# Optimization experiments

Hardware: AMD Instinct MI355X
Metric: run time of the kernel (lower is better)

The kernel has to match this reference:

```python
import jax, jax.numpy as jnp
import numpy as np

B, N, M = 64, 1025, 1024          # N = M + 1 (node 0 is the zero-padding node)
TREE_FEAT = 96
QVEC = 95                          # sum(range(10)) + 10*5
IN_CH = TREE_FEAT + 32             # tree features + q_conv output
EPS = 1e-5


def _tree_conv(x, idx, W, b):
    # x: (B, C, N); idx: (B, 3M) child-triple indices into node axis
    g = jnp.take_along_axis(x, idx[:, None, :], axis=2)        # (B, C, 3M)
    Bn, C, L = g.shape
    g = g.reshape(Bn, C, L // 3, 3)                            # (B, C, M, 3)
    out = jnp.einsum('bcmk,ock->bom', g, W) + b[None, :, None] # Conv1d k=3 s=3
    zero = jnp.zeros((Bn, W.shape[0], 1), out.dtype)           # re-prepend zero node
    return jnp.concatenate([zero, out], axis=2)                # (B, O, M+1)


def _tree_norm(x):
    # TreeLayerNorm: per-sample mean/std over (channels, nodes); torch.std is unbiased
    mean = jnp.mean(x, axis=(1, 2), keepdims=True)
    std = jnp.std(x, axis=(1, 2), keepdims=True, ddof=1)
    return (x - mean) / (std + EPS)


def setup_inputs() -> dict:
    key = jax.random.key(0)
    ks = jax.random.split(key, 17)
    p = lambda k, s: jax.random.normal(k, s, dtype=jnp.float32) * 0.05
    return {
        'q_vecs': jax.random.normal(ks[0], (B, QVEC), dtype=jnp.float32),
        'trees': jax.random.normal(ks[1], (B, N, TREE_FEAT), dtype=jnp.float32),
        'idxes': jax.random.randint(ks[2], (B, 3 * M), 0, N),
        # q_conv: Linear(95,64) -> Linear(64,128) -> Linear(128,64) -> Linear(64,32)
        'Wq1': p(ks[3], (QVEC, 64)),  'bq1': jnp.zeros((64,), jnp.float32),
        'Wq2': p(ks[4], (64, 128)),   'bq2': jnp.zeros((128,), jnp.float32),
        'Wq3': p(ks[5], (128, 64)),   'bq3': jnp.zeros((64,), jnp.float32),
        'Wq4': p(ks[6], (64, 32)),    'bq4': jnp.zeros((32,), jnp.float32),
        # tree_conv kernels: (out, in, 3)
        'Wc1': p(ks[7], (512, IN_CH, 3)), 'bc1': jnp.zeros((512,), jnp.float32),
        'Wc2': p(ks[8], (256, 512, 3)),   'bc2': jnp.zeros((256,), jnp.float32),
        'Wc3': p(ks[9], (128, 256, 3)),   'bc3': jnp.zeros((128,), jnp.float32),
    }


def reference(q_vecs, trees, idxes,
              Wq1, bq1, Wq2, bq2, Wq3, bq3, Wq4, bq4,
              Wc1, bc1, Wc2, bc2, Wc3, bc3):
    # q_conv: 4 stacked linears (no nonlinearity between them in the source)
    q = q_vecs @ Wq1 + bq1
    q = q @ Wq2 + bq2
    q = q @ Wq3 + bq3
    q = q @ Wq4 + bq4                                    # (B, 32)

    Bn, Nn = trees.shape[:2]
    q_rep = jnp.broadcast_to(q[:, None, :], (Bn, Nn, q.shape[-1]))
    aug = jnp.concatenate([trees, q_rep], axis=2)        # (B, N, IN_CH)
    x = jnp.transpose(aug, (0, 2, 1))                    # (B, IN_CH, N)

    x = _tree_conv(x, idxes, Wc1, bc1)
    x = jax.nn.leaky_relu(_tree_norm(x), negative_slope=0.01)
    x = _tree_conv(x, idxes, Wc2, bc2)
    x = jax.nn.leaky_relu(_tree_norm(x), negative_slope=0.01)
    x = _tree_conv(x, idxes, Wc3, bc3)
    x = _tree_norm(x)
    return jnp.max(x, axis=2)                            # DynamicPooling -> (B, 128)
```

## Files before the change

kernel.cpp:

```cpp
#include <hip/hip_runtime.h>
#include <hip/hip_bf16.h>

typedef __attribute__((ext_vector_type(8))) short short8;
typedef __attribute__((ext_vector_type(4))) float f32x4;

#define EPSV 1e-5f

__device__ __forceinline__ float bf2f(ushort u){
  union { uint i; float f; } x; x.i = ((uint)u) << 16; return x.f;
}
__device__ __forceinline__ ushort f2bf(float f){
  union { float f; uint i; } x; x.f = f;
  uint r = (x.i + 0x7FFFu + ((x.i >> 16) & 1u)) >> 16;
  return (ushort)r;
}

__global__ void init_kernel(ushort* x1, float* stats, int* maxbuf){
  int i = blockIdx.x * 256 + threadIdx.x;
  if (i < 384)  stats[i] = 0.f;
  if (i < 8192) maxbuf[i] = 0;
  if (i < 32768){ int b = i >> 9, c = i & 511; x1[(size_t)b*1025*512 + c] = 0; }
}

__global__ void zero2_kernel(ushort* x2){
  int i = blockIdx.x * 256 + threadIdx.x;
  int b = i >> 8, c = i & 255;
  x2[(size_t)b*1025*256 + c] = 0;
}

__global__ void qconv_kernel(const float* __restrict__ qv,
    const float* __restrict__ W1, const float* __restrict__ b1,
    const float* __restrict__ W2, const float* __restrict__ b2,
    const float* __restrict__ W3, const float* __restrict__ b3,
    const float* __restrict__ W4, const float* __restrict__ b4,
    float* __restrict__ qout){
  __shared__ float v0[96], h1[64], h2[128], h3[64];
  int b = blockIdx.x, t = threadIdx.x;
  if (t < 95) v0[t] = qv[b*95 + t];
  __syncthreads();
  if (t < 64){ float s = b1[t]; for (int i=0;i<95;i++)  s += v0[i]*W1[i*64 + t];  h1[t]=s; }
  __syncthreads();
  if (t < 128){ float s = b2[t]; for (int i=0;i<64;i++)  s += h1[i]*W2[i*128 + t]; h2[t]=s; }
  __syncthreads();
  if (t < 64){ float s = b3[t]; for (int i=0;i<128;i++) s += h2[i]*W3[i*64 + t];  h3[t]=s; }
  __syncthreads();
  if (t < 32){ float s = b4[t]; for (int i=0;i<64;i++)  s += h3[i]*W4[i*32 + t];  qout[b*32 + t]=s; }
}

__global__ void aug_kernel(const float* __restrict__ trees, const float* __restrict__ q,
                           ushort* __restrict__ aug){
  int n = blockIdx.x;
  int b = blockIdx.y;
  int c = threadIdx.x;
  float v = (c < 96) ? trees[((size_t)b*1025 + n)*96 + c] : q[b*32 + (c - 96)];
  aug[(((size_t)b*1025 + n) << 7) + c] = f2bf(v);
}

__global__ void prepw_kernel(const float* __restrict__ wc, ushort* __restrict__ wt,
                             int O, int C){
  int i = blockIdx.x * 256 + threadIdx.x;
  int total = O * 3 * C;
  if (i >= total) return;
  int o  = i / (3*C);
  int K  = i - o*3*C;
  int kp = K / C;
  int c  = K - kp*C;
  wt[i] = f2bf(wc[(o*C + c)*3 + kp]);
}

template<int CIN, int GY, bool DO_MAX>
__global__ __launch_bounds__(256) void conv_kernel(
    const ushort* __restrict__ xin, const ushort* __restrict__ wt,
    const float* __restrict__ bias, const int* __restrict__ idxes,
    ushort* __restrict__ xout, float* __restrict__ stats, int* __restrict__ maxbuf){
  constexpr int K3   = 3 * CIN;
  constexpr int NT   = K3 / 32;
  constexpr int COUT = GY * 128;
  constexpr int NWG  = 8 * GY * 64;

  const int bid  = blockIdx.x;
  const int wu   = (bid & 7) * (NWG >> 3) + (bid >> 3);
  const int m0   = (wu & 7) * 128;
  const int rest = wu >> 3;
  const int o0   = (rest % GY) * 128;
  const int b    = rest / GY;

  const int t = threadIdx.x;
  const int lane = t & 63, wid = t >> 6;
  const int WM = (wid & 1) * 64, WO = (wid >> 1) * 64;
  const int fr = lane & 15, fg = lane >> 4;
  const int fc = (fg ^ ((fr >> 1) & 3)) * 8;

  __shared__ __align__(16) union {
    struct { ushort A[2][128][32]; ushort B[2][128][32]; } s;
    ushort stage[128][132];
  } sh;
  __shared__ int idx_s[384];

  for (int i = t; i < 384; i += 256) idx_s[i] = idxes[b*3072 + m0*3 + i];
  __syncthreads();

  const int r = t >> 1, h = t & 1, sx = (r >> 1) & 3;
  const int p0 = ((2*h)     ^ sx) * 8;
  const int p1 = ((2*h + 1) ^ sx) * 8;
  const int n0 = idx_s[r*3 + 0], n1 = idx_s[r*3 + 1], n2 = idx_s[r*3 + 2];
  const ushort* xb   = xin + (size_t)b * 1025 * CIN;
  const ushort* wrow = wt + (size_t)(o0 + r) * K3 + h*16;

  uint4 ra0, ra1, rb0, rb1;
  auto GLOAD = [&](int ch){
    const int k0 = ch * 32;
    const int kp = k0 / CIN;
    const int c0 = k0 - kp * CIN;
    const int node = (kp == 0) ? n0 : (kp == 1) ? n1 : n2;
    const ushort* sa = xb + (size_t)node * CIN + c0 + h*16;
    ra0 = *reinterpret_cast<const uint4*>(sa);
    ra1 = *reinterpret_cast<const uint4*>(sa + 8);
    const ushort* sb = wrow + k0;
    rb0 = *reinterpret_cast<const uint4*>(sb);
    rb1 = *reinterpret_cast<const uint4*>(sb + 8);
  };
  auto DSW = [&](int bf){
    *reinterpret_cast<uint4*>(&sh.s.A[bf][r][p0]) = ra0;
    *reinterpret_cast<uint4*>(&sh.s.A[bf][r][p1]) = ra1;
    *reinterpret_cast<uint4*>(&sh.s.B[bf][r][p0]) = rb0;
    *reinterpret_cast<uint4*>(&sh.s.B[bf][r][p1]) = rb1;
  };

  f32x4 acc[4][4] = {};

  GLOAD(0);
  DSW(0);
  __syncthreads();

  for (int ch = 0; ch < NT; ++ch){
    if (ch + 1 < NT) GLOAD(ch + 1);
    const int cur = ch & 1;
    short8 af[4], bf4[4];
    #pragma unroll
    for (int i = 0; i < 4; ++i){
      af[i]  = *reinterpret_cast<const short8*>(&sh.s.A[cur][WM + i*16 + fr][fc]);
      bf4[i] = *reinterpret_cast<const short8*>(&sh.s.B[cur][WO + i*16 + fr][fc]);
    }
    __builtin_amdgcn_s_setprio(1);
    #pragma unroll
    for (int mf = 0; mf < 4; ++mf)
      #pragma unroll
      for (int nf = 0; nf < 4; ++nf)
        acc[mf][nf] = __builtin_amdgcn_mfma_f32_16x16x32_bf16(af[mf], bf4[nf], acc[mf][nf], 0, 0, 0);
    __builtin_amdgcn_s_setprio(0);
    if (ch + 1 < NT){
      DSW(cur ^ 1);
      __syncthreads();
    }
  }

  float bsv[4];
  #pragma unroll
  for (int nf = 0; nf < 4; ++nf) bsv[nf] = bias[o0 + WO + nf*16 + fr];
  float lsum = 0.f, lsq = 0.f;
  float cmax[4] = { -1e30f, -1e30f, -1e30f, -1e30f };
  #pragma unroll
  for (int mf = 0; mf < 4; ++mf)
    #pragma unroll
    for (int nf = 0; nf < 4; ++nf)
      #pragma unroll
      for (int i = 0; i < 4; ++i){
        float v = acc[mf][nf][i] + bsv[nf];
        lsum += v; lsq += v*v;
        if (DO_MAX) cmax[nf] = fmaxf(cmax[nf], v);
        else acc[mf][nf][i] = v;
      }
  #pragma unroll
  for (int off = 1; off < 64; off <<= 1){
    lsum += __shfl_xor(lsum, off);
    lsq  += __shfl_xor(lsq,  off);
  }
  if (lane == 0){
    atomicAdd(&stats[b],      lsum);
    atomicAdd(&stats[64 + b], lsq);
  }
  if (DO_MAX){
    #pragma unroll
    for (int nf = 0; nf < 4; ++nf){
      float v = cmax[nf];
      v = fmaxf(v, __shfl_xor(v, 16));
      v = fmaxf(v, __shfl_xor(v, 32));
      if (lane < 16)
        atomicMax(&maxbuf[b*COUT + o0 + WO + nf*16 + fr], __float_as_int(v));
    }
  } else {
    __syncthreads();
    #pragma unroll
    for (int mf = 0; mf < 4; ++mf)
      #pragma unroll
      for (int nf = 0; nf < 4; ++nf)
        #pragma unroll
        for (int i = 0; i < 4; ++i)
          sh.stage[WM + mf*16 + fg*4 + i][WO + nf*16 + fr] = f2bf(acc[mf][nf][i]);
    __syncthreads();
    #pragma unroll
    for (int it = 0; it < 16; ++it){
      int row = it*8 + (t >> 5);
      int col = (t & 31) * 4;
      uint2 v = *reinterpret_cast<const uint2*>(&sh.stage[row][col]);
      *reinterpret_cast<uint2*>(xout + ((size_t)(b*1025 + 1 + m0 + row))*COUT + o0 + col) = v;
    }
  }
}

__global__ void norm_kernel(ushort* __restrict__ x, const float* __restrict__ st,
                            float cnt, int nvec_per_b){
  int b = blockIdx.y;
  int j = blockIdx.x * 256 + threadIdx.x;
  if (j >= nvec_per_b) return;
  float sum = st[b], sq = st[64 + b];
  float mean = sum / cnt;
  float var  = fmaxf((sq - sum*sum/cnt) / (cnt - 1.f), 0.f);
  float rs   = 1.f / (sqrtf(var) + EPSV);
  ushort* p = x + ((size_t)b * nvec_per_b + j) * 8;
  union { uint4 v; ushort u[8]; } d;
  d.v = *reinterpret_cast<const uint4*>(p);
  #pragma unroll
  for (int k = 0; k < 8; ++k){
    float f = bf2f(d.u[k]);
    f = (f - mean) * rs;
    f = (f >= 0.f) ? f : 0.01f * f;
    d.u[k] = f2bf(f);
  }
  *reinterpret_cast<uint4*>(p) = d.v;
}

__global__ void final_kernel(const int* __restrict__ maxbuf, const float* __restrict__ st,
                             float* __restrict__ out){
  int i = blockIdx.x * 256 + threadIdx.x;
  int b = i >> 7;
  const float cnt = 131200.f;
  float sum = st[b], sq = st[64 + b];
  float mean = sum / cnt;
  float var  = fmaxf((sq - sum*sum/cnt) / (cnt - 1.f), 0.f);
  float rs   = 1.f / (sqrtf(var) + EPSV);
  out[i] = (__int_as_float(maxbuf[i]) - mean) * rs;
}

static constexpr size_t SZ_X1  = (size_t)64*1025*512*2;
static constexpr size_t SZ_X2  = (size_t)64*1025*256*2;
static constexpr size_t OFF_X1 = 0;
static constexpr size_t OFF_X2 = OFF_X1 + SZ_X1;
static constexpr size_t OFF_AUG = OFF_X2;
static constexpr size_t OFF_WT1 = OFF_X2 + SZ_X2;
static constexpr size_t OFF_WT2 = OFF_WT1 + (size_t)512*384*2;
static constexpr size_t OFF_WT3 = OFF_WT2 + (size_t)256*1536*2;
static constexpr size_t OFF_Q   = OFF_WT3 + (size_t)128*768*2;
static constexpr size_t OFF_ST  = OFF_Q + (size_t)64*32*4;
static constexpr size_t OFF_MAX = OFF_ST + (size_t)384*4;

extern "C" void kernel_launch(void* const* d_in, const int* in_sizes, int n_in,
                              void* d_out, int out_size, void* d_ws, size_t ws_size,
                              hipStream_t stream){
  const float* q_vecs = (const float*)d_in[0];
  const float* trees  = (const float*)d_in[1];
  const int*   idxes  = (const int*)  d_in[2];
  const float* Wq1 = (const float*)d_in[3];  const float* bq1 = (const float*)d_in[4];
  const float* Wq2 = (const float*)d_in[5];  const float* bq2 = (const float*)d_in[6];
  const float* Wq3 = (const float*)d_in[7];  const float* bq3 = (const float*)d_in[8];
  const float* Wq4 = (const float*)d_in[9];  const float* bq4 = (const float*)d_in[10];
  const float* Wc1 = (const float*)d_in[11]; const float* bc1 = (const float*)d_in[12];
  const float* Wc2 = (const float*)d_in[13]; const float* bc2 = (const float*)d_in[14];
  const float* Wc3 = (const float*)d_in[15]; const float* bc3 = (const float*)d_in[16];
  float* out = (float*)d_out;
  char* ws = (char*)d_ws;

  ushort* x1    = (ushort*)(ws + OFF_X1);
  ushort* x2    = (ushort*)(ws + OFF_X2);
  ushort* aug   = (ushort*)(ws + OFF_AUG);
  ushort* wt1   = (ushort*)(ws + OFF_WT1);
  ushort* wt2   = (ushort*)(ws + OFF_WT2);
  ushort* wt3   = (ushort*)(ws + OFF_WT3);
  float*  qbuf  = (float*) (ws + OFF_Q);
  float*  stats = (float*) (ws + OFF_ST);
  int*    maxb  = (int*)   (ws + OFF_MAX);

  init_kernel<<<128, 256, 0, stream>>>(x1, stats, maxb);
  qconv_kernel<<<64, 128, 0, stream>>>(q_vecs, Wq1,bq1, Wq2,bq2, Wq3,bq3, Wq4,bq4, qbuf);
  aug_kernel<<<dim3(1025, 64), 128, 0, stream>>>(trees, qbuf, aug);
  prepw_kernel<<<(512*384 + 255)/256, 256, 0, stream>>>(Wc1, wt1, 512, 128);
  prepw_kernel<<<(256*1536 + 255)/256, 256, 0, stream>>>(Wc2, wt2, 256, 512);
  prepw_kernel<<<(128*768 + 255)/256, 256, 0, stream>>>(Wc3, wt3, 128, 256);

  conv_kernel<128, 4, false><<<2048, 256, 0, stream>>>(aug, wt1, bc1, idxes, x1, stats +   0, nullptr);
  zero2_kernel<<<64, 256, 0, stream>>>(x2);
  norm_kernel<<<dim3((65600 + 255)/256, 64), 256, 0, stream>>>(x1, stats +   0, 524800.f, 65600);
  conv_kernel<512, 2, false><<<1024, 256, 0, stream>>>(x1,  wt2, bc2, idxes, x2, stats + 128, nullptr);
  norm_kernel<<<dim3((32800 + 255)/256, 64), 256, 0, stream>>>(x2, stats + 128, 262400.f, 32800);
  conv_kernel<256, 1, true ><<<512, 256, 0, stream>>>(x2,  wt3, bc3, idxes, nullptr, stats + 256, maxb);
  final_kernel<<<32, 256, 0, stream>>>(maxb, stats + 256, out);
}
```

Baseline: 276.4 us.

## Deepen conv GEMM prefetch to two chunks ahead with dual register buffers

```diff
diff --git a/kernel.cpp b/kernel.cpp
--- a/kernel.cpp
+++ b/kernel.cpp
@@ -75,6 +75,7 @@
     ushort* __restrict__ xout, float* __restrict__ stats, int* __restrict__ maxbuf){
   constexpr int K3   = 3 * CIN;
   constexpr int NT   = K3 / 32;
+  constexpr int LOG2 = (CIN == 128) ? 7 : (CIN == 256) ? 8 : 9;
   constexpr int COUT = GY * 128;
   constexpr int NWG  = 8 * GY * 64;
 
@@ -105,37 +106,51 @@
   const int p1 = ((2*h + 1) ^ sx) * 8;
   const int n0 = idx_s[r*3 + 0], n1 = idx_s[r*3 + 1], n2 = idx_s[r*3 + 2];
   const ushort* xb   = xin + (size_t)b * 1025 * CIN;
+  const ushort* pA0  = xb + (size_t)n0 * CIN + h*16;
+  const ushort* pA1  = xb + (size_t)n1 * CIN + h*16;
+  const ushort* pA2  = xb + (size_t)n2 * CIN + h*16;
   const ushort* wrow = wt + (size_t)(o0 + r) * K3 + h*16;
 
-  uint4 ra0, ra1, rb0, rb1;
-  auto GLOAD = [&](int ch){
+  uint4 a00, a01, b00, b01;
+  uint4 a10, a11, b10, b11;
+
+  auto GLOAD0 = [&](int ch){
     const int k0 = ch * 32;
-    const int kp = k0 / CIN;
-    const int c0 = k0 - kp * CIN;
-    const int node = (kp == 0) ? n0 : (kp == 1) ? n1 : n2;
-    const ushort* sa = xb + (size_t)node * CIN + c0 + h*16;
-    ra0 = *reinterpret_cast<const uint4*>(sa);
-    ra1 = *reinterpret_cast<const uint4*>(sa + 8);
+    const int kp = k0 >> LOG2;
+    const int c0 = k0 - (kp << LOG2);
+    const ushort* sa = ((kp == 0) ? pA0 : (kp == 1) ? pA1 : pA2) + c0;
+    a00 = *reinterpret_cast<const uint4*>(sa);
+    a01 = *reinterpret_cast<const uint4*>(sa + 8);
     const ushort* sb = wrow + k0;
-    rb0 = *reinterpret_cast<const uint4*>(sb);
-    rb1 = *reinterpret_cast<const uint4*>(sb + 8);
-  };
-  auto DSW = [&](int bf){
-    *reinterpret_cast<uint4*>(&sh.s.A[bf][r][p0]) = ra0;
-    *reinterpret_cast<uint4*>(&sh.s.A[bf][r][p1]) = ra1;
-    *reinterpret_cast<uint4*>(&sh.s.B[bf][r][p0]) = rb0;
-    *reinterpret_cast<uint4*>(&sh.s.B[bf][r][p1]) = rb1;
+    b00 = *reinterpret_cast<const uint4*>(sb);
+    b01 = *reinterpret_cast<const uint4*>(sb + 8);
+  };
+  auto GLOAD1 = [&](int ch){
+    const int k0 = ch * 32;
+    const int kp = k0 >> LOG2;
+    const int c0 = k0 - (kp << LOG2);
+    const ushort* sa = ((kp == 0) ? pA0 : (kp == 1) ? pA1 : pA2) + c0;
+    a10 = *reinterpret_cast<const uint4*>(sa);
+    a11 = *reinterpret_cast<const uint4*>(sa + 8);
+    const ushort* sb = wrow + k0;
+    b10 = *reinterpret_cast<const uint4*>(sb);
+    b11 = *reinterpret_cast<const uint4*>(sb + 8);
+  };
+  auto DSW0 = [&](int bf){
+    *reinterpret_cast<uint4*>(&sh.s.A[bf][r][p0]) = a00;
+    *reinterpret_cast<uint4*>(&sh.s.A[bf][r][p1]) = a01;
+    *reinterpret_cast<uint4*>(&sh.s.B[bf][r][p0]) = b00;
+    *reinterpret_cast<uint4*>(&sh.s.B[bf][r][p1]) = b01;
+  };
+  auto DSW1 = [&](int bf){
+    *reinterpret_cast<uint4*>(&sh.s.A[bf][r][p0]) = a10;
+    *reinterpret_cast<uint4*>(&sh.s.A[bf][r][p1]) = a11;
+    *reinterpret_cast<uint4*>(&sh.s.B[bf][r][p0]) = b10;
+    *reinterpret_cast<uint4*>(&sh.s.B[bf][r][p1]) = b11;
   };
 
   f32x4 acc[4][4] = {};
-
-  GLOAD(0);
-  DSW(0);
-  __syncthreads();
-
-  for (int ch = 0; ch < NT; ++ch){
-    if (ch + 1 < NT) GLOAD(ch + 1);
-    const int cur = ch & 1;
+  auto COMPUTE = [&](int cur){
     short8 af[4], bf4[4];
     #pragma unroll
     for (int i = 0; i < 4; ++i){
@@ -149,8 +164,22 @@
       for (int nf = 0; nf < 4; ++nf)
         acc[mf][nf] = __builtin_amdgcn_mfma_f32_16x16x32_bf16(af[mf], bf4[nf], acc[mf][nf], 0, 0, 0);
     __builtin_amdgcn_s_setprio(0);
-    if (ch + 1 < NT){
-      DSW(cur ^ 1);
+  };
+
+  GLOAD0(0);
+  DSW0(0);
+  GLOAD1(1);
+  __syncthreads();
+
+  for (int ch = 0; ch < NT; ch += 2){
+    if (ch + 2 < NT) GLOAD0(ch + 2);
+    COMPUTE(0);
+    DSW1(1);
+    __syncthreads();
+    if (ch + 3 < NT) GLOAD1(ch + 3);
+    COMPUTE(1);
+    if (ch + 2 < NT){
+      DSW0(0);
       __syncthreads();
     }
   }
```

Result: faster. 259.2 us (-6.2%).

## Load weight fragments directly from global memory and drop LDS staging for outputs

Applied to the files above, without the earlier changes.

```diff
diff --git a/kernel.cpp b/kernel.cpp
--- a/kernel.cpp
+++ b/kernel.cpp
@@ -75,6 +75,7 @@
     ushort* __restrict__ xout, float* __restrict__ stats, int* __restrict__ maxbuf){
   constexpr int K3   = 3 * CIN;
   constexpr int NT   = K3 / 32;
+  constexpr int LOG2 = (CIN == 128) ? 7 : (CIN == 256) ? 8 : 9;
   constexpr int COUT = GY * 128;
   constexpr int NWG  = 8 * GY * 64;
 
@@ -91,10 +92,7 @@
   const int fr = lane & 15, fg = lane >> 4;
   const int fc = (fg ^ ((fr >> 1) & 3)) * 8;
 
-  __shared__ __align__(16) union {
-    struct { ushort A[2][128][32]; ushort B[2][128][32]; } s;
-    ushort stage[128][132];
-  } sh;
+  __shared__ __align__(16) ushort As[2][128][32];
   __shared__ int idx_s[384];
 
   for (int i = t; i < 384; i += 256) idx_s[i] = idxes[b*3072 + m0*3 + i];
@@ -104,44 +102,44 @@
   const int p0 = ((2*h)     ^ sx) * 8;
   const int p1 = ((2*h + 1) ^ sx) * 8;
   const int n0 = idx_s[r*3 + 0], n1 = idx_s[r*3 + 1], n2 = idx_s[r*3 + 2];
-  const ushort* xb   = xin + (size_t)b * 1025 * CIN;
-  const ushort* wrow = wt + (size_t)(o0 + r) * K3 + h*16;
-
-  uint4 ra0, ra1, rb0, rb1;
-  auto GLOAD = [&](int ch){
+  const ushort* xb  = xin + (size_t)b * 1025 * CIN;
+  const ushort* pA0 = xb + (size_t)n0 * CIN + h*16;
+  const ushort* pA1 = xb + (size_t)n1 * CIN + h*16;
+  const ushort* pA2 = xb + (size_t)n2 * CIN + h*16;
+  const ushort* wb  = wt + (size_t)(o0 + WO + fr) * K3 + fg*8;
+
+  uint4 ra0, ra1;
+  auto GLOADA = [&](int ch){
     const int k0 = ch * 32;
-    const int kp = k0 / CIN;
-    const int c0 = k0 - kp * CIN;
-    const int node = (kp == 0) ? n0 : (kp == 1) ? n1 : n2;
-    const ushort* sa = xb + (size_t)node * CIN + c0 + h*16;
+    const int kp = k0 >> LOG2;
+    const int c0 = k0 - (kp << LOG2);
+    const ushort* sa = ((kp == 0) ? pA0 : (kp == 1) ? pA1 : pA2) + c0;
     ra0 = *reinterpret_cast<const uint4*>(sa);
     ra1 = *reinterpret_cast<const uint4*>(sa + 8);
-    const ushort* sb = wrow + k0;
-    rb0 = *reinterpret_cast<const uint4*>(sb);
-    rb1 = *reinterpret_cast<const uint4*>(sb + 8);
   };
-  auto DSW = [&](int bf){
-    *reinterpret_cast<uint4*>(&sh.s.A[bf][r][p0]) = ra0;
-    *reinterpret_cast<uint4*>(&sh.s.A[bf][r][p1]) = ra1;
-    *reinterpret_cast<uint4*>(&sh.s.B[bf][r][p0]) = rb0;
-    *reinterpret_cast<uint4*>(&sh.s.B[bf][r][p1]) = rb1;
+  auto DSWA = [&](int bf){
+    *reinterpret_cast<uint4*>(&As[bf][r][p0]) = ra0;
+    *reinterpret_cast<uint4*>(&As[bf][r][p1]) = ra1;
   };
 
   f32x4 acc[4][4] = {};
 
-  GLOAD(0);
-  DSW(0);
+  GLOADA(0);
+  DSWA(0);
   __syncthreads();
 
   for (int ch = 0; ch < NT; ++ch){
-    if (ch + 1 < NT) GLOAD(ch + 1);
+    if (ch + 1 < NT) GLOADA(ch + 1);
+    const ushort* wk = wb + ch * 32;
+    short8 bf4[4];
+    #pragma unroll
+    for (int i = 0; i < 4; ++i)
+      bf4[i] = *reinterpret_cast<const short8*>(wk + (size_t)(i*16) * K3);
     const int cur = ch & 1;
-    short8 af[4], bf4[4];
-    #pragma unroll
-    for (int i = 0; i < 4; ++i){
-      af[i]  = *reinterpret_cast<const short8*>(&sh.s.A[cur][WM + i*16 + fr][fc]);
-      bf4[i] = *reinterpret_cast<const short8*>(&sh.s.B[cur][WO + i*16 + fr][fc]);
-    }
+    short8 af[4];
+    #pragma unroll
+    for (int i = 0; i < 4; ++i)
+      af[i] = *reinterpret_cast<const short8*>(&As[cur][WM + i*16 + fr][fc]);
     __builtin_amdgcn_s_setprio(1);
     #pragma unroll
     for (int mf = 0; mf < 4; ++mf)
@@ -150,7 +148,7 @@
         acc[mf][nf] = __builtin_amdgcn_mfma_f32_16x16x32_bf16(af[mf], bf4[nf], acc[mf][nf], 0, 0, 0);
     __builtin_amdgcn_s_setprio(0);
     if (ch + 1 < NT){
-      DSW(cur ^ 1);
+      DSWA(cur ^ 1);
       __syncthreads();
     }
   }
@@ -190,22 +188,16 @@
         atomicMax(&maxbuf[b*COUT + o0 + WO + nf*16 + fr], __float_as_int(v));
     }
   } else {
-    __syncthreads();
+    ushort* orow = xout + ((size_t)(b*1025 + 1 + m0 + WM + fg*4))*COUT + o0 + WO + fr;
     #pragma unroll
     for (int mf = 0; mf < 4; ++mf)
       #pragma unroll
-      for (int nf = 0; nf < 4; ++nf)
+      for (int i = 0; i < 4; ++i){
+        ushort* pr = orow + (size_t)(mf*16 + i)*COUT;
         #pragma unroll
-        for (int i = 0; i < 4; ++i)
-          sh.stage[WM + mf*16 + fg*4 + i][WO + nf*16 + fr] = f2bf(acc[mf][nf][i]);
-    __syncthreads();
-    #pragma unroll
-    for (int it = 0; it < 16; ++it){
-      int row = it*8 + (t >> 5);
-      int col = (t & 31) * 4;
-      uint2 v = *reinterpret_cast<const uint2*>(&sh.stage[row][col]);
-      *reinterpret_cast<uint2*>(xout + ((size_t)(b*1025 + 1 + m0 + row))*COUT + o0 + col) = v;
-    }
+        for (int nf = 0; nf < 4; ++nf)
+          pr[nf*16] = f2bf(acc[mf][nf][i]);
+      }
   }
 }
 
```

Measured after the change: 351.3 us. 27.1% more time.
